# Kernel tuning notes

Measured on AMD Instinct MI355X. Metric: run time of the kernel, lower is better.

The kernel has to match this reference:

```python
import jax, jax.numpy as jnp
import numpy as np

N = 500000
P = 50000
IN_DIM = 9
H = 128
EPS = 1e-5


def _xavier(key, fan_in, fan_out, gain=0.5):
    std = gain * np.sqrt(2.0 / (fan_in + fan_out))
    return jax.random.normal(key, (fan_in, fan_out), dtype=jnp.float32) * std


def setup_inputs() -> dict:
    key = jax.random.key(0)
    kx, kid, k0, k1, k2 = jax.random.split(key, 5)
    x = jax.random.normal(kx, (N, IN_DIM), dtype=jnp.float32)
    # guarantee every polyline id in [0, P) appears so torch.unique inverse == ids
    ids = jnp.concatenate([jnp.arange(P, dtype=jnp.int64),
                           jax.random.randint(kid, (N - P,), 0, P, dtype=jnp.int64)])
    polyline_ids = jax.random.permutation(kid, ids)
    inp = {"x": x, "polyline_ids": polyline_ids,
           "W0": _xavier(k0, IN_DIM, H), "b0": jnp.zeros((H,), jnp.float32),
           "g0": jnp.ones((H,), jnp.float32), "be0": jnp.zeros((H,), jnp.float32),
           "W1": _xavier(k1, 2 * H, H), "b1": jnp.zeros((H,), jnp.float32),
           "g1": jnp.ones((H,), jnp.float32), "be1": jnp.zeros((H,), jnp.float32),
           "W2": _xavier(k2, 2 * H, H), "b2": jnp.zeros((H,), jnp.float32),
           "g2": jnp.ones((H,), jnp.float32), "be2": jnp.zeros((H,), jnp.float32)}
    return inp


def _encoder(h, W, b, g, be):
    # Linear -> LayerNorm -> ReLU (Dropout is identity in eval)
    z = h @ W + b
    mu = jnp.mean(z, axis=-1, keepdims=True)
    var = jnp.var(z, axis=-1, keepdims=True)
    z = (z - mu) * jax.lax.rsqrt(var + EPS) * g + be
    return jax.nn.relu(z)


def _seg_max(h, ids):
    m = jax.ops.segment_max(h, ids, num_segments=P)
    # torch scatter_reduce(amax, include_self=False) leaves empty rows at 0
    return jnp.where(jnp.isfinite(m), m, 0.0)


def reference(x, polyline_ids, W0, b0, g0, be0, W1, b1, g1, be1, W2, b2, g2, be2):
    ids = polyline_ids.astype(jnp.int32)  # all of [0,P) present -> inverse == ids
    h = _encoder(x, W0, b0, g0, be0)  # [N, H]
    for (W, b, g, be) in ((W1, b1, g1, be1), (W2, b2, g2, be2)):
        agg = _seg_max(h, ids)[ids]               # [N, H] broadcast of per-polyline max
        h = _encoder(jnp.concatenate([h, agg], axis=-1), W, b, g, be)
    polyline_features = _seg_max(h, ids)          # [P, H]
    unique_polylines = jnp.arange(P, dtype=polyline_ids.dtype)
    return polyline_features, unique_polylines
```

## Files before the change

kernel.cpp:

```cpp
#include <hip/hip_runtime.h>
#include <hip/hip_bf16.h>
#include <hip/hip_fp16.h>

#define N_PTS 500000
#define P_POLY 50000
#define IN_DIM 9
#define HDIM 128
#define EPSV 1e-5f
#define BCAP 64
#define NG 7813
#define CAPR 96
#define HS 136

typedef __attribute__((ext_vector_type(8))) short short8;
typedef __attribute__((ext_vector_type(4))) float floatx4;

__device__ __forceinline__ unsigned short f2h(float f) {
  return __half_as_ushort(__float2half(f));
}
__device__ __forceinline__ float h2f(unsigned short u) {
  return __half2float(__ushort_as_half(u));
}
__device__ __forceinline__ unsigned int pkmax(unsigned int a, unsigned int b) {
  unsigned int r;
  asm("v_pk_max_f16 %0, %1, %2" : "=v"(r) : "v"(a), "v"(b));
  return r;
}

__global__ __launch_bounds__(256) void k_bucket(
    const int* __restrict__ ids, unsigned int* __restrict__ cnt, int* __restrict__ list)
{
  int i = blockIdx.x * blockDim.x + threadIdx.x;
  if (i < N_PTS) {
    int id = ids[i];
    unsigned k = atomicAdd(&cnt[id], 1u);
    list[id * BCAP + (k & (BCAP - 1))] = i;
  }
}

__global__ __launch_bounds__(256) void k_scan1(
    const unsigned int* __restrict__ cnt, unsigned int* __restrict__ btot)
{
  __shared__ unsigned int s[256];
  int t = threadIdx.x;
  int i = blockIdx.x * 256 + t;
  s[t] = (i < P_POLY) ? cnt[i] : 0u;
  __syncthreads();
  for (int d = 128; d > 0; d >>= 1) {
    if (t < d) s[t] += s[t + d];
    __syncthreads();
  }
  if (t == 0) btot[blockIdx.x] = s[0];
}

__global__ __launch_bounds__(256) void k_scan2(
    const unsigned int* __restrict__ cnt, const unsigned int* __restrict__ btot,
    const int* __restrict__ list, unsigned int* __restrict__ offsets,
    int* __restrict__ perm, int* __restrict__ gcount, int* __restrict__ gplist)
{
  __shared__ unsigned int s[256];
  __shared__ unsigned int sbase;
  int b = blockIdx.x, t = threadIdx.x;
  int i = b * 256 + t;
  unsigned int v = (i < P_POLY) ? cnt[i] : 0u;
  s[t] = v;
  __syncthreads();
  for (int d = 1; d < 256; d <<= 1) {
    unsigned int tmp = (t >= d) ? s[t - d] : 0u;
    __syncthreads();
    s[t] += tmp;
    __syncthreads();
  }
  unsigned int incl = s[t];
  if (t == 0) {
    unsigned int base = 0;
    for (int j = 0; j < b; ++j) base += btot[j];
    sbase = base;
  }
  __syncthreads();
  unsigned int off = sbase + incl - v;
  if (i < P_POLY) {
    offsets[i] = off;
    unsigned int n = v > BCAP ? (unsigned)BCAP : v;
    int g = (int)(off >> 6);
    int slot = atomicAdd(&gcount[g], 1);
    gplist[g * BCAP + (slot & (BCAP - 1))] = i;
    for (unsigned int k = 0; k < n; ++k)
      perm[off + k] = list[i * BCAP + k];
  }
}

__global__ __launch_bounds__(256) void k_wprep(
    const float* __restrict__ W1, const float* __restrict__ W2,
    unsigned short* __restrict__ Wt1, unsigned short* __restrict__ Wb1,
    unsigned short* __restrict__ Wt2, unsigned short* __restrict__ Wb2)
{
  int idx = blockIdx.x * 256 + threadIdx.x;
  int sel = idx >> 14;
  int e = idx & 16383;
  int c = e & 127;
  int k = e >> 7;
  const float* W = (sel < 2) ? W1 : W2;
  unsigned short* O = sel == 0 ? Wt1 : sel == 1 ? Wb1 : sel == 2 ? Wt2 : Wb2;
  int kg = k + ((sel & 1) ? 128 : 0);
  O[c * 128 + k] = f2h(W[kg * 128 + c]);
}

__device__ __forceinline__ void enc_layer(
    unsigned short* sh, const unsigned short* sagg, const int* pid_loc, char* smisc,
    const unsigned short* __restrict__ Wt, const unsigned short* __restrict__ Wb,
    const float* __restrict__ bias, const float* __restrict__ gamma,
    const float* __restrict__ beta, int w, int l15, int l4, int koff)
{
  const int c0 = w * 32 + l15;
  const int c1 = c0 + 16;
  floatx4 acc[6][2];
#pragma unroll
  for (int mt = 0; mt < 6; ++mt) {
    acc[mt][0] = (floatx4){0.f, 0.f, 0.f, 0.f};
    acc[mt][1] = (floatx4){0.f, 0.f, 0.f, 0.f};
  }
  int pl[6];
#pragma unroll
  for (int mt = 0; mt < 6; ++mt) pl[mt] = pid_loc[mt * 16 + l15];

#pragma unroll
  for (int kk = 0; kk < 4; ++kk) {
    short8 B0 = *reinterpret_cast<const short8*>(Wt + c0 * 128 + kk * 32 + koff);
    short8 B1 = *reinterpret_cast<const short8*>(Wt + c1 * 128 + kk * 32 + koff);
#pragma unroll
    for (int mt = 0; mt < 6; ++mt) {
      short8 a = *reinterpret_cast<const short8*>(sh + (mt * 16 + l15) * HS + kk * 32 + koff);
      acc[mt][0] = __builtin_amdgcn_mfma_f32_16x16x32_f16(a, B0, acc[mt][0], 0, 0, 0);
      acc[mt][1] = __builtin_amdgcn_mfma_f32_16x16x32_f16(a, B1, acc[mt][1], 0, 0, 0);
    }
  }
#pragma unroll
  for (int kk = 0; kk < 4; ++kk) {
    short8 B0 = *reinterpret_cast<const short8*>(Wb + c0 * 128 + kk * 32 + koff);
    short8 B1 = *reinterpret_cast<const short8*>(Wb + c1 * 128 + kk * 32 + koff);
#pragma unroll
    for (int mt = 0; mt < 6; ++mt) {
      short8 a = *reinterpret_cast<const short8*>(sagg + pl[mt] * HS + kk * 32 + koff);
      acc[mt][0] = __builtin_amdgcn_mfma_f32_16x16x32_f16(a, B0, acc[mt][0], 0, 0, 0);
      acc[mt][1] = __builtin_amdgcn_mfma_f32_16x16x32_f16(a, B1, acc[mt][1], 0, 0, 0);
    }
  }

  float bi0 = bias[c0], bi1 = bias[c1];
  float2* part = (float2*)smisc;
  float2* mufin = (float2*)(smisc + 3072);
#pragma unroll
  for (int mt = 0; mt < 6; ++mt) {
    float s[4], ss[4];
#pragma unroll
    for (int r = 0; r < 4; ++r) {
      float z0 = acc[mt][0][r] + bi0;
      float z1 = acc[mt][1][r] + bi1;
      acc[mt][0][r] = z0;
      acc[mt][1][r] = z1;
      s[r] = z0 + z1;
      ss[r] = fmaf(z0, z0, z1 * z1);
    }
#pragma unroll
    for (int m = 1; m <= 8; m <<= 1) {
#pragma unroll
      for (int r = 0; r < 4; ++r) {
        s[r] += __shfl_xor(s[r], m);
        ss[r] += __shfl_xor(ss[r], m);
      }
    }
    if (l15 == 0) {
#pragma unroll
      for (int r = 0; r < 4; ++r)
        part[w * CAPR + mt * 16 + l4 * 4 + r] = make_float2(s[r], ss[r]);
    }
  }
  __syncthreads();
  if (threadIdx.x < CAPR) {
    int rr = threadIdx.x;
    float2 qa = part[0 * CAPR + rr], qb = part[1 * CAPR + rr];
    float2 qc = part[2 * CAPR + rr], qd = part[3 * CAPR + rr];
    float S = qa.x + qb.x + qc.x + qd.x;
    float SS = qa.y + qb.y + qc.y + qd.y;
    float mu = S * (1.f / 128.f);
    float rv = rsqrtf(SS * (1.f / 128.f) - mu * mu + EPSV);
    mufin[rr] = make_float2(mu, rv);
  }
  __syncthreads();
  float ga0 = gamma[c0], ga1 = gamma[c1], bt0 = beta[c0], bt1 = beta[c1];
#pragma unroll
  for (int mt = 0; mt < 6; ++mt) {
#pragma unroll
    for (int r = 0; r < 4; ++r) {
      int row = mt * 16 + l4 * 4 + r;
      float2 q = mufin[row];
      float v0 = fmaxf(fmaf((acc[mt][0][r] - q.x) * q.y, ga0, bt0), 0.f);
      float v1 = fmaxf(fmaf((acc[mt][1][r] - q.x) * q.y, ga1, bt1), 0.f);
      sh[row * HS + c0] = f2h(v0);
      sh[row * HS + c1] = f2h(v1);
    }
  }
  __syncthreads();
}

__device__ __forceinline__ unsigned int slot_max(
    const unsigned short* sh, int ls, int n, int lane)
{
  const unsigned short* base = sh + ls * HS + 2 * lane;
  unsigned int m = 0u;
  for (int k = 0; k < n; k += 8) {
    unsigned int v[8];
#pragma unroll
    for (int j = 0; j < 8; ++j) {
      int kk = k + j;
      kk = kk < n - 1 ? kk : n - 1;
      v[j] = *reinterpret_cast<const unsigned int*>(base + kk * HS);
    }
    unsigned int a = pkmax(v[0], v[1]);
    unsigned int b = pkmax(v[2], v[3]);
    unsigned int c = pkmax(v[4], v[5]);
    unsigned int d = pkmax(v[6], v[7]);
    m = pkmax(m, pkmax(pkmax(a, b), pkmax(c, d)));
  }
  return m;
}

__global__ __launch_bounds__(256, 3) void k_fused(
    const float* __restrict__ x, const int* __restrict__ perm,
    const unsigned int* __restrict__ cnt, const unsigned int* __restrict__ offsets,
    const int* __restrict__ gcount, const int* __restrict__ gplist,
    const float* __restrict__ W0, const float* __restrict__ b0,
    const float* __restrict__ g0, const float* __restrict__ be0,
    const unsigned short* __restrict__ Wt1, const unsigned short* __restrict__ Wb1,
    const float* __restrict__ b1, const float* __restrict__ g1, const float* __restrict__ be1,
    const unsigned short* __restrict__ Wt2, const unsigned short* __restrict__ Wb2,
    const float* __restrict__ b2, const float* __restrict__ g2, const float* __restrict__ be2,
    float* __restrict__ out)
{
  __shared__ unsigned short sh[CAPR * HS];
  __shared__ unsigned short sagg[BCAP * HS];
  __shared__ char smisc[3840];
  __shared__ short sl_off[BCAP], sl_n[BCAP];
  __shared__ int sl_p[BCAP];
  __shared__ int pid_loc[CAPR];
  __shared__ int s_rs, s_nrows;

  const int g = blockIdx.x;
  const int npoly0 = gcount[g];
  if (npoly0 <= 0) return;
  const int npoly = npoly0 > BCAP ? BCAP : npoly0;
  const int tid = threadIdx.x;
  const int lane = tid & 63;
  const int w = tid >> 6;
  const int l15 = lane & 15;
  const int l4 = lane >> 4;
  const int koff = l4 * 8;

  if (tid < 64) {
    int s = tid;
    int off = 0x7FFFFFFF, n = 0, end = 0, p = 0;
    if (s < npoly) {
      p = gplist[g * BCAP + s];
      off = (int)offsets[p];
      n = (int)cnt[p];
      if (n > BCAP) n = BCAP;
      end = off + n;
    }
    int rsv = off, rev = end;
#pragma unroll
    for (int m = 32; m >= 1; m >>= 1) {
      rsv = min(rsv, __shfl_xor(rsv, m));
      rev = max(rev, __shfl_xor(rev, m));
    }
    if (s == 0) { s_rs = rsv; s_nrows = min(rev - rsv, CAPR); }
    if (s < npoly) {
      int ls = off - rsv;
      sl_off[s] = (short)ls;
      sl_n[s] = (short)n;
      sl_p[s] = p;
      for (int k = 0; k < n; ++k)
        if (ls + k < CAPR) pid_loc[ls + k] = s;
    }
    int nr = min(rev - rsv, CAPR);
    for (int r = nr + s; r < CAPR; r += 64) pid_loc[r] = 0;
  }
  __syncthreads();
  const int rs = s_rs;
  const int nrows = s_nrows;

  float* xs = (float*)smisc;
  for (int e = tid; e < nrows * IN_DIM; e += 256) {
    int r = e / IN_DIM;
    int k = e - r * IN_DIM;
    unsigned o = (unsigned)perm[rs + r];
    if (o >= N_PTS) o = 0;
    xs[e] = x[(size_t)o * IN_DIM + k];
  }
  __syncthreads();

  {
    float w0a[9], w0b[9];
#pragma unroll
    for (int k = 0; k < 9; ++k) {
      float2 t = *reinterpret_cast<const float2*>(W0 + k * 128 + 2 * lane);
      w0a[k] = t.x;
      w0b[k] = t.y;
    }
    float2 bb = *reinterpret_cast<const float2*>(b0 + 2 * lane);
    float2 gg = *reinterpret_cast<const float2*>(g0 + 2 * lane);
    float2 ee = *reinterpret_cast<const float2*>(be0 + 2 * lane);
#pragma unroll
    for (int it = 0; it < 6; ++it) {
      float z0[4], z1[4], s[4], ss[4];
      int rr[4];
#pragma unroll
      for (int u = 0; u < 4; ++u) {
        int r = w + 4 * (it * 4 + u);
        rr[u] = r;
        int rc = r < nrows ? r : 0;
        float a = bb.x, b = bb.y;
#pragma unroll
        for (int k = 0; k < 9; ++k) {
          float xv = xs[rc * 9 + k];
          a = fmaf(xv, w0a[k], a);
          b = fmaf(xv, w0b[k], b);
        }
        z0[u] = a;
        z1[u] = b;
        s[u] = a + b;
        ss[u] = fmaf(a, a, b * b);
      }
#pragma unroll
      for (int m = 1; m <= 32; m <<= 1) {
#pragma unroll
        for (int u = 0; u < 4; ++u) {
          s[u] += __shfl_xor(s[u], m);
          ss[u] += __shfl_xor(ss[u], m);
        }
      }
#pragma unroll
      for (int u = 0; u < 4; ++u) {
        if (rr[u] < nrows) {
          float mu = s[u] * (1.f / 128.f);
          float rv = rsqrtf(ss[u] * (1.f / 128.f) - mu * mu + EPSV);
          float v0 = fmaxf(fmaf((z0[u] - mu) * rv, gg.x, ee.x), 0.f);
          float v1 = fmaxf(fmaf((z1[u] - mu) * rv, gg.y, ee.y), 0.f);
          *reinterpret_cast<ushort2*>(sh + rr[u] * HS + 2 * lane) =
              make_ushort2(f2h(v0), f2h(v1));
        }
      }
    }
  }
  __syncthreads();

  for (int s = w; s < npoly; s += 4) {
    unsigned int m = slot_max(sh, sl_off[s], sl_n[s], lane);
    *reinterpret_cast<unsigned int*>(sagg + s * HS + 2 * lane) = m;
  }
  __syncthreads();

  enc_layer(sh, sagg, pid_loc, smisc, Wt1, Wb1, b1, g1, be1, w, l15, l4, koff);

  for (int s = w; s < npoly; s += 4) {
    unsigned int m = slot_max(sh, sl_off[s], sl_n[s], lane);
    *reinterpret_cast<unsigned int*>(sagg + s * HS + 2 * lane) = m;
  }
  __syncthreads();

  enc_layer(sh, sagg, pid_loc, smisc, Wt2, Wb2, b2, g2, be2, w, l15, l4, koff);

  for (int s = w; s < npoly; s += 4) {
    unsigned int m = slot_max(sh, sl_off[s], sl_n[s], lane);
    float2 f = make_float2(h2f((unsigned short)(m & 0xFFFFu)),
                           h2f((unsigned short)(m >> 16)));
    int p = sl_p[s];
    *reinterpret_cast<float2*>(out + (size_t)p * 128 + 2 * lane) = f;
    if (lane == 0) out[(size_t)P_POLY * 128 + p] = (float)p;
  }
}

#define WS_CNT   0
#define WS_OFF   204800
#define WS_BTOT  409600
#define WS_PERM  413696
#define WS_LIST  2413696
#define WS_GCNT  15213696
#define WS_GPL   15246464
#define WS_W     17247360
#define WS_NEED  17378432

__device__ __attribute__((aligned(256))) unsigned char g_fallback[WS_NEED];

extern "C" void kernel_launch(void* const* d_in, const int* in_sizes, int n_in,
                              void* d_out, int out_size, void* d_ws, size_t ws_size,
                              hipStream_t stream) {
  const float* x = (const float*)d_in[0];
  const int* ids = (const int*)d_in[1];
  const float* W0 = (const float*)d_in[2];
  const float* b0 = (const float*)d_in[3];
  const float* g0 = (const float*)d_in[4];
  const float* be0 = (const float*)d_in[5];
  const float* W1 = (const float*)d_in[6];
  const float* b1 = (const float*)d_in[7];
  const float* g1 = (const float*)d_in[8];
  const float* be1 = (const float*)d_in[9];
  const float* W2 = (const float*)d_in[10];
  const float* b2 = (const float*)d_in[11];
  const float* g2 = (const float*)d_in[12];
  const float* be2 = (const float*)d_in[13];

  char* ws = (char*)d_ws;
  if (ws_size < (size_t)WS_NEED) {
    void* p = nullptr;
    hipGetSymbolAddress(&p, HIP_SYMBOL(g_fallback));
    ws = (char*)p;
  }
  unsigned int* cnt = (unsigned int*)(ws + WS_CNT);
  unsigned int* offsets = (unsigned int*)(ws + WS_OFF);
  unsigned int* btot = (unsigned int*)(ws + WS_BTOT);
  int* perm = (int*)(ws + WS_PERM);
  int* list = (int*)(ws + WS_LIST);
  int* gcount = (int*)(ws + WS_GCNT);
  int* gplist = (int*)(ws + WS_GPL);
  unsigned short* Wt1 = (unsigned short*)(ws + WS_W);
  unsigned short* Wb1 = (unsigned short*)(ws + WS_W + 32768);
  unsigned short* Wt2 = (unsigned short*)(ws + WS_W + 65536);
  unsigned short* Wb2 = (unsigned short*)(ws + WS_W + 98304);
  float* out = (float*)d_out;

  hipMemsetAsync(cnt, 0, P_POLY * 4, stream);
  hipMemsetAsync(gcount, 0, 32768, stream);

  k_bucket<<<(N_PTS + 255) / 256, 256, 0, stream>>>(ids, cnt, list);
  k_scan1<<<196, 256, 0, stream>>>(cnt, btot);
  k_scan2<<<196, 256, 0, stream>>>(cnt, btot, list, offsets, perm, gcount, gplist);
  k_wprep<<<256, 256, 0, stream>>>(W1, W2, Wt1, Wb1, Wt2, Wb2);
  k_fused<<<NG, 256, 0, stream>>>(x, perm, cnt, offsets, gcount, gplist,
                                  W0, b0, g0, be0,
                                  Wt1, Wb1, b1, g1, be1,
                                  Wt2, Wb2, b2, g2, be2, out);
}
```

Before: 512.3 us.

## Replace bucket lists with counting-sort placement and derive block polylines from offsets

The per-id fixed-capacity bucket list and per-group polyline lists are dropped in favour of a count, scan, and atomic placement pass that writes a sorted perm plus per-row polyline ids. The fused kernel now works out its polyline range directly from pid_perm and offsets, which removes the gcount/gplist bookkeeping and the large list workspace. Weight prep is folded into the scan launch, and the MFMA and LayerNorm tiles are skipped past nrows. Occupancy is raised to 4 blocks per CU by shrinking the shared slot arrays, at the cost of an extra kernel pass over ids and a limit of 32 polylines per block.

```diff
diff --git a/kernel.cpp b/kernel.cpp
--- a/kernel.cpp
+++ b/kernel.cpp
@@ -7,9 +7,9 @@
 #define IN_DIM 9
 #define HDIM 128
 #define EPSV 1e-5f
-#define BCAP 64
 #define NG 7813
 #define CAPR 96
+#define SLOTS 32
 #define HS 136
 
 typedef __attribute__((ext_vector_type(8))) short short8;
@@ -27,36 +27,50 @@
   return r;
 }
 
-__global__ __launch_bounds__(256) void k_bucket(
-    const int* __restrict__ ids, unsigned int* __restrict__ cnt, int* __restrict__ list)
+__global__ __launch_bounds__(256) void k_count(
+    const int* __restrict__ ids, unsigned int* __restrict__ cnt)
 {
   int i = blockIdx.x * blockDim.x + threadIdx.x;
-  if (i < N_PTS) {
-    int id = ids[i];
-    unsigned k = atomicAdd(&cnt[id], 1u);
-    list[id * BCAP + (k & (BCAP - 1))] = i;
-  }
-}
-
-__global__ __launch_bounds__(256) void k_scan1(
-    const unsigned int* __restrict__ cnt, unsigned int* __restrict__ btot)
-{
-  __shared__ unsigned int s[256];
-  int t = threadIdx.x;
-  int i = blockIdx.x * 256 + t;
-  s[t] = (i < P_POLY) ? cnt[i] : 0u;
-  __syncthreads();
-  for (int d = 128; d > 0; d >>= 1) {
-    if (t < d) s[t] += s[t + d];
+  if (i < N_PTS) atomicAdd(&cnt[ids[i]], 1u);
+}
+
+__global__ __launch_bounds__(256) void k_scanwp(
+    const unsigned int* __restrict__ cnt, unsigned int* __restrict__ btot,
+    const float* __restrict__ W1, const float* __restrict__ W2,
+    unsigned short* __restrict__ Wt1, unsigned short* __restrict__ Wb1,
+    unsigned short* __restrict__ Wt2, unsigned short* __restrict__ Wb2)
+{
+  if (blockIdx.x < 196) {
+    __shared__ unsigned int s[256];
+    int t = threadIdx.x;
+    int i = blockIdx.x * 256 + t;
+    s[t] = (i < P_POLY) ? cnt[i] : 0u;
     __syncthreads();
-  }
-  if (t == 0) btot[blockIdx.x] = s[0];
+    for (int d = 128; d > 0; d >>= 1) {
+      if (t < d) s[t] += s[t + d];
+      __syncthreads();
+    }
+    if (t == 0) btot[blockIdx.x] = s[0];
+  } else {
+    int bw = blockIdx.x - 196;
+#pragma unroll
+    for (int t = 0; t < 2; ++t) {
+      int idx = (bw * 2 + t) * 256 + threadIdx.x;
+      int sel = idx >> 14;
+      int e = idx & 16383;
+      int c = e & 127;
+      int k = e >> 7;
+      const float* W = (sel < 2) ? W1 : W2;
+      unsigned short* O = sel == 0 ? Wt1 : sel == 1 ? Wb1 : sel == 2 ? Wt2 : Wb2;
+      int kg = k + ((sel & 1) ? 128 : 0);
+      O[c * 128 + k] = f2h(W[kg * 128 + c]);
+    }
+  }
 }
 
 __global__ __launch_bounds__(256) void k_scan2(
     const unsigned int* __restrict__ cnt, const unsigned int* __restrict__ btot,
-    const int* __restrict__ list, unsigned int* __restrict__ offsets,
-    int* __restrict__ perm, int* __restrict__ gcount, int* __restrict__ gplist)
+    unsigned int* __restrict__ offsets, unsigned int* __restrict__ woff)
 {
   __shared__ unsigned int s[256];
   __shared__ unsigned int sbase;
@@ -81,39 +95,32 @@
   unsigned int off = sbase + incl - v;
   if (i < P_POLY) {
     offsets[i] = off;
-    unsigned int n = v > BCAP ? (unsigned)BCAP : v;
-    int g = (int)(off >> 6);
-    int slot = atomicAdd(&gcount[g], 1);
-    gplist[g * BCAP + (slot & (BCAP - 1))] = i;
-    for (unsigned int k = 0; k < n; ++k)
-      perm[off + k] = list[i * BCAP + k];
-  }
-}
-
-__global__ __launch_bounds__(256) void k_wprep(
-    const float* __restrict__ W1, const float* __restrict__ W2,
-    unsigned short* __restrict__ Wt1, unsigned short* __restrict__ Wb1,
-    unsigned short* __restrict__ Wt2, unsigned short* __restrict__ Wb2)
-{
-  int idx = blockIdx.x * 256 + threadIdx.x;
-  int sel = idx >> 14;
-  int e = idx & 16383;
-  int c = e & 127;
-  int k = e >> 7;
-  const float* W = (sel < 2) ? W1 : W2;
-  unsigned short* O = sel == 0 ? Wt1 : sel == 1 ? Wb1 : sel == 2 ? Wt2 : Wb2;
-  int kg = k + ((sel & 1) ? 128 : 0);
-  O[c * 128 + k] = f2h(W[kg * 128 + c]);
+    woff[i] = off;
+  }
+}
+
+__global__ __launch_bounds__(256) void k_place(
+    const int* __restrict__ ids, unsigned int* __restrict__ woff,
+    int* __restrict__ perm, int* __restrict__ pid_perm)
+{
+  int i = blockIdx.x * blockDim.x + threadIdx.x;
+  if (i < N_PTS) {
+    int id = ids[i];
+    unsigned pos = atomicAdd(&woff[id], 1u);
+    perm[pos] = i;
+    pid_perm[pos] = id;
+  }
 }
 
 __device__ __forceinline__ void enc_layer(
     unsigned short* sh, const unsigned short* sagg, const int* pid_loc, char* smisc,
     const unsigned short* __restrict__ Wt, const unsigned short* __restrict__ Wb,
     const float* __restrict__ bias, const float* __restrict__ gamma,
-    const float* __restrict__ beta, int w, int l15, int l4, int koff)
+    const float* __restrict__ beta, int w, int l15, int l4, int koff, int nrows)
 {
   const int c0 = w * 32 + l15;
   const int c1 = c0 + 16;
+  const int mtmax = (nrows + 15) >> 4;
   floatx4 acc[6][2];
 #pragma unroll
   for (int mt = 0; mt < 6; ++mt) {
@@ -130,9 +137,11 @@
     short8 B1 = *reinterpret_cast<const short8*>(Wt + c1 * 128 + kk * 32 + koff);
 #pragma unroll
     for (int mt = 0; mt < 6; ++mt) {
-      short8 a = *reinterpret_cast<const short8*>(sh + (mt * 16 + l15) * HS + kk * 32 + koff);
-      acc[mt][0] = __builtin_amdgcn_mfma_f32_16x16x32_f16(a, B0, acc[mt][0], 0, 0, 0);
-      acc[mt][1] = __builtin_amdgcn_mfma_f32_16x16x32_f16(a, B1, acc[mt][1], 0, 0, 0);
+      if (mt < mtmax) {
+        short8 a = *reinterpret_cast<const short8*>(sh + (mt * 16 + l15) * HS + kk * 32 + koff);
+        acc[mt][0] = __builtin_amdgcn_mfma_f32_16x16x32_f16(a, B0, acc[mt][0], 0, 0, 0);
+        acc[mt][1] = __builtin_amdgcn_mfma_f32_16x16x32_f16(a, B1, acc[mt][1], 0, 0, 0);
+      }
     }
   }
 #pragma unroll
@@ -141,9 +150,11 @@
     short8 B1 = *reinterpret_cast<const short8*>(Wb + c1 * 128 + kk * 32 + koff);
 #pragma unroll
     for (int mt = 0; mt < 6; ++mt) {
-      short8 a = *reinterpret_cast<const short8*>(sagg + pl[mt] * HS + kk * 32 + koff);
-      acc[mt][0] = __builtin_amdgcn_mfma_f32_16x16x32_f16(a, B0, acc[mt][0], 0, 0, 0);
-      acc[mt][1] = __builtin_amdgcn_mfma_f32_16x16x32_f16(a, B1, acc[mt][1], 0, 0, 0);
+      if (mt < mtmax) {
+        short8 a = *reinterpret_cast<const short8*>(sagg + pl[mt] * HS + kk * 32 + koff);
+        acc[mt][0] = __builtin_amdgcn_mfma_f32_16x16x32_f16(a, B0, acc[mt][0], 0, 0, 0);
+        acc[mt][1] = __builtin_amdgcn_mfma_f32_16x16x32_f16(a, B1, acc[mt][1], 0, 0, 0);
+      }
     }
   }
 
@@ -152,28 +163,30 @@
   float2* mufin = (float2*)(smisc + 3072);
 #pragma unroll
   for (int mt = 0; mt < 6; ++mt) {
-    float s[4], ss[4];
-#pragma unroll
-    for (int r = 0; r < 4; ++r) {
-      float z0 = acc[mt][0][r] + bi0;
-      float z1 = acc[mt][1][r] + bi1;
-      acc[mt][0][r] = z0;
-      acc[mt][1][r] = z1;
-      s[r] = z0 + z1;
-      ss[r] = fmaf(z0, z0, z1 * z1);
-    }
-#pragma unroll
-    for (int m = 1; m <= 8; m <<= 1) {
+    if (mt < mtmax) {
+      float s[4], ss[4];
 #pragma unroll
       for (int r = 0; r < 4; ++r) {
-        s[r] += __shfl_xor(s[r], m);
-        ss[r] += __shfl_xor(ss[r], m);
-      }
-    }
-    if (l15 == 0) {
-#pragma unroll
-      for (int r = 0; r < 4; ++r)
-        part[w * CAPR + mt * 16 + l4 * 4 + r] = make_float2(s[r], ss[r]);
+        float z0 = acc[mt][0][r] + bi0;
+        float z1 = acc[mt][1][r] + bi1;
+        acc[mt][0][r] = z0;
+        acc[mt][1][r] = z1;
+        s[r] = z0 + z1;
+        ss[r] = fmaf(z0, z0, z1 * z1);
+      }
+#pragma unroll
+      for (int m = 1; m <= 8; m <<= 1) {
+#pragma unroll
+        for (int r = 0; r < 4; ++r) {
+          s[r] += __shfl_xor(s[r], m);
+          ss[r] += __shfl_xor(ss[r], m);
+        }
+      }
+      if (l15 == 0) {
+#pragma unroll
+        for (int r = 0; r < 4; ++r)
+          part[w * CAPR + mt * 16 + l4 * 4 + r] = make_float2(s[r], ss[r]);
+      }
     }
   }
   __syncthreads();
@@ -191,14 +204,16 @@
   float ga0 = gamma[c0], ga1 = gamma[c1], bt0 = beta[c0], bt1 = beta[c1];
 #pragma unroll
   for (int mt = 0; mt < 6; ++mt) {
-#pragma unroll
-    for (int r = 0; r < 4; ++r) {
-      int row = mt * 16 + l4 * 4 + r;
-      float2 q = mufin[row];
-      float v0 = fmaxf(fmaf((acc[mt][0][r] - q.x) * q.y, ga0, bt0), 0.f);
-      float v1 = fmaxf(fmaf((acc[mt][1][r] - q.x) * q.y, ga1, bt1), 0.f);
-      sh[row * HS + c0] = f2h(v0);
-      sh[row * HS + c1] = f2h(v1);
+    if (mt < mtmax) {
+#pragma unroll
+      for (int r = 0; r < 4; ++r) {
+        int row = mt * 16 + l4 * 4 + r;
+        float2 q = mufin[row];
+        float v0 = fmaxf(fmaf((acc[mt][0][r] - q.x) * q.y, ga0, bt0), 0.f);
+        float v1 = fmaxf(fmaf((acc[mt][1][r] - q.x) * q.y, ga1, bt1), 0.f);
+        sh[row * HS + c0] = f2h(v0);
+        sh[row * HS + c1] = f2h(v1);
+      }
     }
   }
   __syncthreads();
@@ -226,10 +241,9 @@
   return m;
 }
 
-__global__ __launch_bounds__(256, 3) void k_fused(
+__global__ __launch_bounds__(256, 4) void k_fused(
     const float* __restrict__ x, const int* __restrict__ perm,
-    const unsigned int* __restrict__ cnt, const unsigned int* __restrict__ offsets,
-    const int* __restrict__ gcount, const int* __restrict__ gplist,
+    const int* __restrict__ pid_perm, const unsigned int* __restrict__ offsets,
     const float* __restrict__ W0, const float* __restrict__ b0,
     const float* __restrict__ g0, const float* __restrict__ be0,
     const unsigned short* __restrict__ Wt1, const unsigned short* __restrict__ Wb1,
@@ -239,17 +253,33 @@
     float* __restrict__ out)
 {
   __shared__ unsigned short sh[CAPR * HS];
-  __shared__ unsigned short sagg[BCAP * HS];
+  __shared__ unsigned short sagg[SLOTS * HS];
   __shared__ char smisc[3840];
-  __shared__ short sl_off[BCAP], sl_n[BCAP];
-  __shared__ int sl_p[BCAP];
+  __shared__ short sl_off[SLOTS], sl_n[SLOTS];
   __shared__ int pid_loc[CAPR];
-  __shared__ int s_rs, s_nrows;
 
   const int g = blockIdx.x;
-  const int npoly0 = gcount[g];
-  if (npoly0 <= 0) return;
-  const int npoly = npoly0 > BCAP ? BCAP : npoly0;
+  const int j1 = g * 64;
+  const int j2 = j1 + 64;
+
+  int q = pid_perm[j1];
+  int p_lo = q + ((int)offsets[q] < j1 ? 1 : 0);
+  int p_hi, endrow;
+  if (j2 >= N_PTS) {
+    p_hi = P_POLY - 1;
+    endrow = N_PTS;
+  } else {
+    int q2 = pid_perm[j2];
+    p_hi = ((int)offsets[q2] < j2) ? q2 : q2 - 1;
+    endrow = (p_hi + 1 < P_POLY) ? (int)offsets[p_hi + 1] : N_PTS;
+  }
+  int npoly = p_hi - p_lo + 1;
+  if (npoly <= 0) return;
+  if (npoly > SLOTS) npoly = SLOTS;
+  const int rs = (int)offsets[p_lo];
+  int nrows = endrow - rs;
+  if (nrows > CAPR) nrows = CAPR;
+
   const int tid = threadIdx.x;
   const int lane = tid & 63;
   const int w = tid >> 6;
@@ -257,45 +287,29 @@
   const int l4 = lane >> 4;
   const int koff = l4 * 8;
 
-  if (tid < 64) {
-    int s = tid;
-    int off = 0x7FFFFFFF, n = 0, end = 0, p = 0;
-    if (s < npoly) {
-      p = gplist[g * BCAP + s];
-      off = (int)offsets[p];
-      n = (int)cnt[p];
-      if (n > BCAP) n = BCAP;
-      end = off + n;
-    }
-    int rsv = off, rev = end;
-#pragma unroll
-    for (int m = 32; m >= 1; m >>= 1) {
-      rsv = min(rsv, __shfl_xor(rsv, m));
-      rev = max(rev, __shfl_xor(rev, m));
-    }
-    if (s == 0) { s_rs = rsv; s_nrows = min(rev - rsv, CAPR); }
-    if (s < npoly) {
-      int ls = off - rsv;
-      sl_off[s] = (short)ls;
-      sl_n[s] = (short)n;
-      sl_p[s] = p;
-      for (int k = 0; k < n; ++k)
-        if (ls + k < CAPR) pid_loc[ls + k] = s;
-    }
-    int nr = min(rev - rsv, CAPR);
-    for (int r = nr + s; r < CAPR; r += 64) pid_loc[r] = 0;
-  }
-  __syncthreads();
-  const int rs = s_rs;
-  const int nrows = s_nrows;
-
   float* xs = (float*)smisc;
   for (int e = tid; e < nrows * IN_DIM; e += 256) {
     int r = e / IN_DIM;
     int k = e - r * IN_DIM;
-    unsigned o = (unsigned)perm[rs + r];
-    if (o >= N_PTS) o = 0;
-    xs[e] = x[(size_t)o * IN_DIM + k];
+    xs[e] = x[(size_t)perm[rs + r] * IN_DIM + k];
+  }
+  for (int s = tid; s < npoly; s += 256) {
+    int o = (int)offsets[p_lo + s];
+    int e2 = (p_lo + s + 1 < P_POLY) ? (int)offsets[p_lo + s + 1] : N_PTS;
+    int ls = o - rs;
+    int n = e2 - o;
+    if (n > CAPR - ls) n = CAPR - ls;
+    sl_off[s] = (short)ls;
+    sl_n[s] = (short)n;
+  }
+  for (int r = tid; r < CAPR; r += 256) {
+    int v = 0;
+    if (r < nrows) {
+      v = pid_perm[rs + r] - p_lo;
+      if (v >= SLOTS) v = SLOTS - 1;
+      if (v < 0) v = 0;
+    }
+    pid_loc[r] = v;
   }
   __syncthreads();
 
@@ -312,42 +326,44 @@
     float2 ee = *reinterpret_cast<const float2*>(be0 + 2 * lane);
 #pragma unroll
     for (int it = 0; it < 6; ++it) {
-      float z0[4], z1[4], s[4], ss[4];
-      int rr[4];
-#pragma unroll
-      for (int u = 0; u < 4; ++u) {
-        int r = w + 4 * (it * 4 + u);
-        rr[u] = r;
-        int rc = r < nrows ? r : 0;
-        float a = bb.x, b = bb.y;
-#pragma unroll
-        for (int k = 0; k < 9; ++k) {
-          float xv = xs[rc * 9 + k];
-          a = fmaf(xv, w0a[k], a);
-          b = fmaf(xv, w0b[k], b);
+      if (it * 16 < nrows) {
+        float z0[4], z1[4], s[4], ss[4];
+        int rr[4];
+#pragma unroll
+        for (int u = 0; u < 4; ++u) {
+          int r = w + 4 * (it * 4 + u);
+          rr[u] = r;
+          int rc = r < nrows ? r : 0;
+          float a = bb.x, b = bb.y;
+#pragma unroll
+          for (int k = 0; k < 9; ++k) {
+            float xv = xs[rc * 9 + k];
+            a = fmaf(xv, w0a[k], a);
+            b = fmaf(xv, w0b[k], b);
+          }
+          z0[u] = a;
+          z1[u] = b;
+          s[u] = a + b;
+          ss[u] = fmaf(a, a, b * b);
         }
-        z0[u] = a;
-        z1[u] = b;
-        s[u] = a + b;
-        ss[u] = fmaf(a, a, b * b);
-      }
-#pragma unroll
-      for (int m = 1; m <= 32; m <<= 1) {
+#pragma unroll
+        for (int m = 1; m <= 32; m <<= 1) {
+#pragma unroll
+          for (int u = 0; u < 4; ++u) {
+            s[u] += __shfl_xor(s[u], m);
+            ss[u] += __shfl_xor(ss[u], m);
+          }
+        }
 #pragma unroll
         for (int u = 0; u < 4; ++u) {
-          s[u] += __shfl_xor(s[u], m);
-          ss[u] += __shfl_xor(ss[u], m);
-        }
-      }
-#pragma unroll
-      for (int u = 0; u < 4; ++u) {
-        if (rr[u] < nrows) {
-          float mu = s[u] * (1.f / 128.f);
-          float rv = rsqrtf(ss[u] * (1.f / 128.f) - mu * mu + EPSV);
-          float v0 = fmaxf(fmaf((z0[u] - mu) * rv, gg.x, ee.x), 0.f);
-          float v1 = fmaxf(fmaf((z1[u] - mu) * rv, gg.y, ee.y), 0.f);
-          *reinterpret_cast<ushort2*>(sh + rr[u] * HS + 2 * lane) =
-              make_ushort2(f2h(v0), f2h(v1));
+          if (rr[u] < nrows) {
+            float mu = s[u] * (1.f / 128.f);
+            float rv = rsqrtf(ss[u] * (1.f / 128.f) - mu * mu + EPSV);
+            float v0 = fmaxf(fmaf((z0[u] - mu) * rv, gg.x, ee.x), 0.f);
+            float v1 = fmaxf(fmaf((z1[u] - mu) * rv, gg.y, ee.y), 0.f);
+            *reinterpret_cast<ushort2*>(sh + rr[u] * HS + 2 * lane) =
+                make_ushort2(f2h(v0), f2h(v1));
+          }
         }
       }
     }
@@ -360,7 +376,7 @@
   }
   __syncthreads();
 
-  enc_layer(sh, sagg, pid_loc, smisc, Wt1, Wb1, b1, g1, be1, w, l15, l4, koff);
+  enc_layer(sh, sagg, pid_loc, smisc, Wt1, Wb1, b1, g1, be1, w, l15, l4, koff, nrows);
 
   for (int s = w; s < npoly; s += 4) {
     unsigned int m = slot_max(sh, sl_off[s], sl_n[s], lane);
@@ -368,13 +384,13 @@
   }
   __syncthreads();
 
-  enc_layer(sh, sagg, pid_loc, smisc, Wt2, Wb2, b2, g2, be2, w, l15, l4, koff);
+  enc_layer(sh, sagg, pid_loc, smisc, Wt2, Wb2, b2, g2, be2, w, l15, l4, koff, nrows);
 
   for (int s = w; s < npoly; s += 4) {
     unsigned int m = slot_max(sh, sl_off[s], sl_n[s], lane);
     float2 f = make_float2(h2f((unsigned short)(m & 0xFFFFu)),
                            h2f((unsigned short)(m >> 16)));
-    int p = sl_p[s];
+    int p = p_lo + s;
     *reinterpret_cast<float2*>(out + (size_t)p * 128 + 2 * lane) = f;
     if (lane == 0) out[(size_t)P_POLY * 128 + p] = (float)p;
   }
@@ -382,13 +398,12 @@
 
 #define WS_CNT   0
 #define WS_OFF   204800
-#define WS_BTOT  409600
-#define WS_PERM  413696
-#define WS_LIST  2413696
-#define WS_GCNT  15213696
-#define WS_GPL   15246464
-#define WS_W     17247360
-#define WS_NEED  17378432
+#define WS_WOFF  409600
+#define WS_BTOT  614400
+#define WS_PERM  618496
+#define WS_PID   2618496
+#define WS_W     4618496
+#define WS_NEED  4749568
 
 __device__ __attribute__((aligned(256))) unsigned char g_fallback[WS_NEED];
 
@@ -418,11 +433,10 @@
   }
   unsigned int* cnt = (unsigned int*)(ws + WS_CNT);
   unsigned int* offsets = (unsigned int*)(ws + WS_OFF);
+  unsigned int* woff = (unsigned int*)(ws + WS_WOFF);
   unsigned int* btot = (unsigned int*)(ws + WS_BTOT);
   int* perm = (int*)(ws + WS_PERM);
-  int* list = (int*)(ws + WS_LIST);
-  int* gcount = (int*)(ws + WS_GCNT);
-  int* gplist = (int*)(ws + WS_GPL);
+  int* pid_perm = (int*)(ws + WS_PID);
   unsigned short* Wt1 = (unsigned short*)(ws + WS_W);
   unsigned short* Wb1 = (unsigned short*)(ws + WS_W + 32768);
   unsigned short* Wt2 = (unsigned short*)(ws + WS_W + 65536);
@@ -430,13 +444,11 @@
   float* out = (float*)d_out;
 
   hipMemsetAsync(cnt, 0, P_POLY * 4, stream);
-  hipMemsetAsync(gcount, 0, 32768, stream);
-
-  k_bucket<<<(N_PTS + 255) / 256, 256, 0, stream>>>(ids, cnt, list);
-  k_scan1<<<196, 256, 0, stream>>>(cnt, btot);
-  k_scan2<<<196, 256, 0, stream>>>(cnt, btot, list, offsets, perm, gcount, gplist);
-  k_wprep<<<256, 256, 0, stream>>>(W1, W2, Wt1, Wb1, Wt2, Wb2);
-  k_fused<<<NG, 256, 0, stream>>>(x, perm, cnt, offsets, gcount, gplist,
+  k_count<<<(N_PTS + 255) / 256, 256, 0, stream>>>(ids, cnt);
+  k_scanwp<<<324, 256, 0, stream>>>(cnt, btot, W1, W2, Wt1, Wb1, Wt2, Wb2);
+  k_scan2<<<196, 256, 0, stream>>>(cnt, btot, offsets, woff);
+  k_place<<<(N_PTS + 255) / 256, 256, 0, stream>>>(ids, woff, perm, pid_perm);
+  k_fused<<<NG, 256, 0, stream>>>(x, perm, pid_perm, offsets,
                                   W0, b0, g0, be0,
                                   Wt1, Wb1, b1, g1, be1,
                                   Wt2, Wb2, b2, g2, be2, out);
```

Result: faster. 442.6 us (-13.6%).
